# Performance work log

Measured on AMD Instinct MI355X. Metric: run time of the kernel, lower is better.

## Reference

```python
import jax, jax.numpy as jnp
import numpy as np

_CH = [(3,64),(64,64),(64,128),(128,128),(128,256),(256,256),(256,256),(256,512),(512,512),(512,512),(512,512),(512,512),(512,512)]
_RES = [32,32,16,16,8,8,8,4,4,4,2,2,2]
# (conv index, pool index applied after, or None)
_PLAN = [(0,None),(1,0),(2,None),(3,1),(4,None),(5,None),(6,2),(7,None),(8,None),(9,3),(10,None),(11,None),(12,4)]


def _bilinear(x, py, px):
    # x: [B,C,H,W]; py/px: [B,K2,H,W] float sampling coords (zero-padded outside)
    B, C, H, W = x.shape
    y0 = jnp.floor(py); x0 = jnp.floor(px)
    wy1 = (py - y0)[:, None]  # [B,1,K2,H,W]
    wx1 = (px - x0)[:, None]
    xf = x.reshape(B, C, H * W)

    def gather(yi, xi):
        valid = ((yi >= 0) & (yi < H) & (xi >= 0) & (xi < W)).astype(x.dtype)
        idx = (jnp.clip(yi, 0, H - 1) * W + jnp.clip(xi, 0, W - 1)).astype(jnp.int32)
        def gb(xb, ib, vb):
            return xb[:, ib.reshape(-1)].reshape((xb.shape[0],) + ib.shape) * vb[None]
        return jax.vmap(gb)(xf, idx, valid)  # [B,C,K2,H,W]

    g00 = gather(y0, x0); g01 = gather(y0, x0 + 1)
    g10 = gather(y0 + 1, x0); g11 = gather(y0 + 1, x0 + 1)
    return (g00 * (1 - wy1) * (1 - wx1) + g01 * (1 - wy1) * wx1
            + g10 * wy1 * (1 - wx1) + g11 * wy1 * wx1)


def _deform_conv(x, offset, w, b):
    # torchvision-style DeformConv2d, stride 1, padding 1, 3x3 kernel
    B, C, H, W = x.shape
    K = w.shape[-1]
    off = offset.reshape(B, K * K, 2, H, W)  # per kernel tap: (dy, dx)
    kk = jnp.arange(K, dtype=x.dtype) - (K // 2)
    ky = jnp.repeat(kk, K); kx = jnp.tile(kk, K)  # [K2]
    py = jnp.arange(H, dtype=x.dtype)[None, None, :, None] + ky[None, :, None, None] + off[:, :, 0]
    px = jnp.arange(W, dtype=x.dtype)[None, None, None, :] + kx[None, :, None, None] + off[:, :, 1]
    s = _bilinear(x, py, px)  # [B,C,K2,H,W]
    out = jnp.einsum('bckhw,ock->bohw', s, w.reshape(w.shape[0], C, K * K))
    return out + b[None, :, None, None]


def _bn_relu(x, g, beta):
    # training-mode BatchNorm2d (batch statistics, eps=1e-5) + ReLU
    m = jnp.mean(x, axis=(0, 2, 3), keepdims=True)
    v = jnp.mean((x - m) ** 2, axis=(0, 2, 3), keepdims=True)
    xn = (x - m) * jax.lax.rsqrt(v + 1e-5)
    return jax.nn.relu(xn * g[None, :, None, None] + beta[None, :, None, None])


def _deform_pool(x, perm, new_perm):
    # permutation-indexed 2x2 max pool: gather by perm, pool, re-permute output
    B, C, H, W = x.shape
    xp = x.reshape(B, C, H * W)[:, :, perm].reshape(B, C, H, W)
    p = xp.reshape(B, C, H // 2, 2, W // 2, 2).max(axis=(3, 5))
    return p.reshape(B, C, (H // 2) * (W // 2))[:, :, new_perm].reshape(B, C, H // 2, W // 2)


def _forward(x, offs, ws, bs, gs, betas, perms, nperms, fws, fbs):
    for ci, pi in _PLAN:
        x = _deform_conv(x, offs[ci], ws[ci], bs[ci])
        x = _bn_relu(x, gs[ci], betas[ci])
        if pi is not None:
            x = _deform_pool(x, perms[pi], nperms[pi])
    h = x.reshape(x.shape[0], -1)  # [B,512]
    h = jax.nn.relu(h @ fws[0].T + fbs[0])
    h = jax.nn.relu(h @ fws[1].T + fbs[1])
    return h @ fws[2].T + fbs[2]


def setup_inputs() -> dict:
    key = jax.random.key(0)
    ks = iter(jax.random.split(key, 128))
    B = 32
    d = {"x": jax.random.normal(next(ks), (B, 3, 32, 32), jnp.float32)}
    for i, ((ci, co), r) in enumerate(zip(_CH, _RES), 1):
        d[f"off{i}"] = jax.random.normal(next(ks), (B, 18, r, r), jnp.float32) * 0.5
        d[f"w{i}"] = jax.random.normal(next(ks), (co, ci, 3, 3), jnp.float32) * (1.0 / np.sqrt(ci * 9))
        d[f"b{i}"] = jnp.zeros((co,), jnp.float32)
        d[f"g{i}"] = jnp.ones((co,), jnp.float32)
        d[f"bb{i}"] = jnp.zeros((co,), jnp.float32)
    for i, r in enumerate([32, 16, 8, 4, 2], 1):
        d[f"perm{i}"] = jax.random.permutation(next(ks), r * r)
        d[f"nperm{i}"] = jax.random.permutation(next(ks), (r // 2) * (r // 2))
    for i, (di, do) in enumerate([(512, 4096), (4096, 4096), (4096, 100)], 1):
        d[f"fw{i}"] = jax.random.normal(next(ks), (do, di), jnp.float32) * (1.0 / np.sqrt(di))
        d[f"fb{i}"] = jnp.zeros((do,), jnp.float32)
    return d


def reference(x,
              off1, off2, off3, off4, off5, off6, off7, off8, off9, off10, off11, off12, off13,
              w1, w2, w3, w4, w5, w6, w7, w8, w9, w10, w11, w12, w13,
              b1, b2, b3, b4, b5, b6, b7, b8, b9, b10, b11, b12, b13,
              g1, g2, g3, g4, g5, g6, g7, g8, g9, g10, g11, g12, g13,
              bb1, bb2, bb3, bb4, bb5, bb6, bb7, bb8, bb9, bb10, bb11, bb12, bb13,
              perm1, perm2, perm3, perm4, perm5,
              nperm1, nperm2, nperm3, nperm4, nperm5,
              fw1, fb1, fw2, fb2, fw3, fb3):
    offs = [off1, off2, off3, off4, off5, off6, off7, off8, off9, off10, off11, off12, off13]
    ws = [w1, w2, w3, w4, w5, w6, w7, w8, w9, w10, w11, w12, w13]
    bs = [b1, b2, b3, b4, b5, b6, b7, b8, b9, b10, b11, b12, b13]
    gs = [g1, g2, g3, g4, g5, g6, g7, g8, g9, g10, g11, g12, g13]
    betas = [bb1, bb2, bb3, bb4, bb5, bb6, bb7, bb8, bb9, bb10, bb11, bb12, bb13]
    perms = [perm1, perm2, perm3, perm4, perm5]
    nperms = [nperm1, nperm2, nperm3, nperm4, nperm5]
    return _forward(x, offs, ws, bs, gs, betas, perms, nperms, [fw1, fw2, fw3], [fb1, fb2, fb3])
```

## Files before the change

### kernel.cpp

```cpp
#include <hip/hip_runtime.h>
#include <hip/hip_bf16.h>

typedef __hip_bfloat16 bf16;
typedef __attribute__((ext_vector_type(8))) short short8;
typedef __attribute__((ext_vector_type(4))) float f32x4;
typedef unsigned short u16;
#define BF2F(x) __bfloat162float(x)

__device__ __forceinline__ u16 f2bfbits(float v) {
  bf16 h = __float2bfloat16(v);
  return *(u16*)&h;
}
__device__ __forceinline__ float bfbits2f(u16 u) {
  bf16 h; *(u16*)&h = u;
  return BF2F(h);
}
__device__ __forceinline__ void splitbf(float v, u16& hi, u16& lo) {
  hi = f2bfbits(v);
  lo = f2bfbits(v - bfbits2f(hi));
}

union VecU {
  u16 u[8];
  short8 s;
};

__global__ void nchw2nhwc_kernel(const float* __restrict__ in, float* __restrict__ out,
                                 int B, int C, int HW) {
  int i = blockIdx.x * blockDim.x + threadIdx.x;
  int total = B * C * HW;
  if (i >= total) return;
  int c = i % C; int p = (i / C) % HW; int b = i / (C * HW);
  out[i] = in[((size_t)b * C + c) * HW + p];
}

template<int C, int Kp>
__device__ __forceinline__ void wtc_pair(const float* __restrict__ w, u16* __restrict__ Wh,
                                         u16* __restrict__ Wl, int rel) {
  int co = rel / C, ci = rel % C;
  const float* src = w + ((size_t)co * C + ci) * 9;
  float v[9];
#pragma unroll
  for (int k2 = 0; k2 < 9; ++k2) v[k2] = src[k2];
  size_t ob = (size_t)co * Kp + ci;
#pragma unroll
  for (int k2 = 0; k2 < 9; ++k2) {
    u16 hh, ll; splitbf(v[k2], hh, ll);
    Wh[ob + (size_t)k2 * C] = hh;
    Wl[ob + (size_t)k2 * C] = ll;
  }
}

#define PAIR_TOTAL 1634496
#define PAD_TOTAL 320

__global__ void wtc_all_v2(
    const float* w0, const float* w1, const float* w2, const float* w3,
    const float* w4, const float* w5, const float* w6, const float* w7,
    const float* w8, const float* w9, const float* w10, const float* w11,
    const float* w12, u16* __restrict__ Wh, u16* __restrict__ Wl) {
  int i = blockIdx.x * blockDim.x + threadIdx.x;
  if (i >= PAIR_TOTAL + PAD_TOTAL) return;
  if (i >= PAIR_TOTAL) {
    int t = i - PAIR_TOTAL;
    int co = t / 5, k = 27 + t % 5;
    int o = co * 32 + k;
    Wh[o] = 0; Wl[o] = 0;
    return;
  }
  if      (i < 192)     wtc_pair<3, 32>(w0, Wh + 0, Wl + 0, i);
  else if (i < 4288)    wtc_pair<64, 576>(w1, Wh + 2048, Wl + 2048, i - 192);
  else if (i < 12480)   wtc_pair<64, 576>(w2, Wh + 38912, Wl + 38912, i - 4288);
  else if (i < 28864)   wtc_pair<128, 1152>(w3, Wh + 112640, Wl + 112640, i - 12480);
  else if (i < 61632)   wtc_pair<128, 1152>(w4, Wh + 260096, Wl + 260096, i - 28864);
  else if (i < 127168)  wtc_pair<256, 2304>(w5, Wh + 555008, Wl + 555008, i - 61632);
  else if (i < 192704)  wtc_pair<256, 2304>(w6, Wh + 1144832, Wl + 1144832, i - 127168);
  else if (i < 323776)  wtc_pair<256, 2304>(w7, Wh + 1734656, Wl + 1734656, i - 192704);
  else if (i < 585920)  wtc_pair<512, 4608>(w8, Wh + 2914304, Wl + 2914304, i - 323776);
  else if (i < 848064)  wtc_pair<512, 4608>(w9, Wh + 5273600, Wl + 5273600, i - 585920);
  else if (i < 1110208) wtc_pair<512, 4608>(w10, Wh + 7632896, Wl + 7632896, i - 848064);
  else if (i < 1372352) wtc_pair<512, 4608>(w11, Wh + 9992192, Wl + 9992192, i - 1110208);
  else                  wtc_pair<512, 4608>(w12, Wh + 12351488, Wl + 12351488, i - 1372352);
}

__global__ void act_convert(const float* __restrict__ x,
                            u16* __restrict__ Ah, u16* __restrict__ Al, int total) {
  int i = blockIdx.x * blockDim.x + threadIdx.x;
  if (i >= total) return;
  u16 hh, ll; splitbf(x[i], hh, ll);
  Ah[i] = hh; Al[i] = ll;
}

__global__ __launch_bounds__(256) void deform_sample_scalar(
    const float* __restrict__ act, const float* __restrict__ off,
    u16* __restrict__ Sh, u16* __restrict__ Sl,
    int m0, int Mc, int B, int H, int W, int C, int Kp) {
  int i = blockIdx.x * blockDim.x + threadIdx.x;
  int total = Mc * Kp;
  if (i >= total) return;
  int kp = i % Kp;
  int ml = i / Kp;
  float val = 0.f;
  int K = 9 * C;
  if (kp < K) {
    int c = kp % C; int k2 = kp / C;
    int m = m0 + ml;
    int HW = H * W;
    int b = m / HW; int p = m - b * HW; int y = p / W; int x = p - y * W;
    size_t ob = (size_t)b * 18 * HW + p;
    float dy = off[ob + (size_t)(2 * k2) * HW];
    float dx = off[ob + (size_t)(2 * k2 + 1) * HW];
    float py = (float)(y + k2 / 3 - 1) + dy;
    float px = (float)(x + k2 % 3 - 1) + dx;
    float y0f = floorf(py), x0f = floorf(px);
    float wy = py - y0f, wx = px - x0f;
    int iy0 = (int)y0f, ix0 = (int)x0f;
    int iy1 = iy0 + 1, ix1 = ix0 + 1;
    float w00 = (1.f - wy) * (1.f - wx), w01 = (1.f - wy) * wx;
    float w10 = wy * (1.f - wx), w11 = wy * wx;
    if (iy0 < 0 || iy0 >= H) { w00 = 0.f; w01 = 0.f; }
    if (iy1 < 0 || iy1 >= H) { w10 = 0.f; w11 = 0.f; }
    if (ix0 < 0 || ix0 >= W) { w00 = 0.f; w10 = 0.f; }
    if (ix1 < 0 || ix1 >= W) { w01 = 0.f; w11 = 0.f; }
    int cy0 = min(max(iy0, 0), H - 1), cy1 = min(max(iy1, 0), H - 1);
    int cx0 = min(max(ix0, 0), W - 1), cx1 = min(max(ix1, 0), W - 1);
    size_t rowb = (size_t)b * HW;
    float v00 = act[(rowb + cy0 * W + cx0) * C + c];
    float v01 = act[(rowb + cy0 * W + cx1) * C + c];
    float v10 = act[(rowb + cy1 * W + cx0) * C + c];
    float v11 = act[(rowb + cy1 * W + cx1) * C + c];
    val = w00 * v00 + w01 * v01 + w10 * v10 + w11 * v11;
  }
  u16 hh, ll; splitbf(val, hh, ll);
  size_t base = (size_t)ml * Kp + kp;
  Sh[base] = hh; Sl[base] = ll;
}

#define LDA 40

__global__ __launch_bounds__(256) void mfma_gemm_tiled(
    const u16* __restrict__ Ah, const u16* __restrict__ Al,
    const u16* __restrict__ Bh, const u16* __restrict__ Bl,
    float* __restrict__ Cf, int M, int N, int Kp, int kPerZ, int splitMode) {
  __shared__ __align__(16) u16 lds[2 * 4 * 64 * LDA];
  const int TS = 64 * LDA;
  const int BS = 4 * TS;
  int tid = threadIdx.x;
  int lane = tid & 63, wave = tid >> 6;
  int l15 = lane & 15, quad = lane >> 4;
  int wr = wave >> 1, wc = wave & 1;
  int m0 = blockIdx.x * 64, n0 = blockIdx.y * 64;
  int kStart = blockIdx.z * kPerZ;
  int kEnd = min(Kp, kStart + kPerZ);
  int nSteps = (kEnd - kStart) >> 5;

  int sr = tid >> 2, sc = (tid & 3) << 3;
  const u16* gAh = Ah + (size_t)(m0 + sr) * Kp + kStart + sc;
  const u16* gAl = Al + (size_t)(m0 + sr) * Kp + kStart + sc;
  const u16* gBh = Bh + (size_t)(n0 + sr) * Kp + kStart + sc;
  const u16* gBl = Bl + (size_t)(n0 + sr) * Kp + kStart + sc;
  int soff = sr * LDA + sc;

  f32x4 z4 = {0.f, 0.f, 0.f, 0.f};
  f32x4 acc00 = z4, acc01 = z4, acc10 = z4, acc11 = z4;

  {
    short8 a = *(const short8*)gAh;
    short8 b = *(const short8*)gAl;
    short8 c = *(const short8*)gBh;
    short8 d = *(const short8*)gBl;
    *(short8*)&lds[0 * TS + soff] = a;
    *(short8*)&lds[1 * TS + soff] = b;
    *(short8*)&lds[2 * TS + soff] = c;
    *(short8*)&lds[3 * TS + soff] = d;
  }
  __syncthreads();

  int raoff = (wr * 32 + l15) * LDA + quad * 8;
  int rboff = (wc * 32 + l15) * LDA + quad * 8;

  for (int i = 0; i < nSteps; ++i) {
    int cb = (i & 1) * BS;
    bool hasNext = (i + 1 < nSteps);
    short8 nA, nB, nC, nD;
    if (hasNext) {
      int kn = (i + 1) << 5;
      nA = *(const short8*)(gAh + kn);
      nB = *(const short8*)(gAl + kn);
      nC = *(const short8*)(gBh + kn);
      nD = *(const short8*)(gBl + kn);
    }
    short8 ah0 = *(const short8*)&lds[cb + 0 * TS + raoff];
    short8 ah1 = *(const short8*)&lds[cb + 0 * TS + raoff + 16 * LDA];
    short8 al0 = *(const short8*)&lds[cb + 1 * TS + raoff];
    short8 al1 = *(const short8*)&lds[cb + 1 * TS + raoff + 16 * LDA];
    short8 bh0 = *(const short8*)&lds[cb + 2 * TS + rboff];
    short8 bh1 = *(const short8*)&lds[cb + 2 * TS + rboff + 16 * LDA];
    short8 bl0 = *(const short8*)&lds[cb + 3 * TS + rboff];
    short8 bl1 = *(const short8*)&lds[cb + 3 * TS + rboff + 16 * LDA];
    acc00 = __builtin_amdgcn_mfma_f32_16x16x32_bf16(ah0, bh0, acc00, 0, 0, 0);
    acc01 = __builtin_amdgcn_mfma_f32_16x16x32_bf16(ah0, bh1, acc01, 0, 0, 0);
    acc10 = __builtin_amdgcn_mfma_f32_16x16x32_bf16(ah1, bh0, acc10, 0, 0, 0);
    acc11 = __builtin_amdgcn_mfma_f32_16x16x32_bf16(ah1, bh1, acc11, 0, 0, 0);
    acc00 = __builtin_amdgcn_mfma_f32_16x16x32_bf16(ah0, bl0, acc00, 0, 0, 0);
    acc01 = __builtin_amdgcn_mfma_f32_16x16x32_bf16(ah0, bl1, acc01, 0, 0, 0);
    acc10 = __builtin_amdgcn_mfma_f32_16x16x32_bf16(ah1, bl0, acc10, 0, 0, 0);
    acc11 = __builtin_amdgcn_mfma_f32_16x16x32_bf16(ah1, bl1, acc11, 0, 0, 0);
    acc00 = __builtin_amdgcn_mfma_f32_16x16x32_bf16(al0, bh0, acc00, 0, 0, 0);
    acc01 = __builtin_amdgcn_mfma_f32_16x16x32_bf16(al0, bh1, acc01, 0, 0, 0);
    acc10 = __builtin_amdgcn_mfma_f32_16x16x32_bf16(al1, bh0, acc10, 0, 0, 0);
    acc11 = __builtin_amdgcn_mfma_f32_16x16x32_bf16(al1, bh1, acc11, 0, 0, 0);
    if (hasNext) {
      int ob = cb ^ BS;
      *(short8*)&lds[ob + 0 * TS + soff] = nA;
      *(short8*)&lds[ob + 1 * TS + soff] = nB;
      *(short8*)&lds[ob + 2 * TS + soff] = nC;
      *(short8*)&lds[ob + 3 * TS + soff] = nD;
      __syncthreads();
    }
  }

  float* out = Cf + (splitMode ? (size_t)blockIdx.z * M * N : (size_t)0);
  f32x4 av[2][2] = {{acc00, acc01}, {acc10, acc11}};
#pragma unroll
  for (int t = 0; t < 2; ++t) {
    int mB = m0 + wr * 32 + t * 16 + (quad << 2);
#pragma unroll
    for (int u = 0; u < 2; ++u) {
      int n = n0 + wc * 32 + u * 16 + l15;
      f32x4 a = av[t][u];
#pragma unroll
      for (int reg = 0; reg < 4; ++reg) {
        int m = mB + reg;
        out[(size_t)m * N + n] = a[reg];
      }
    }
  }
}

__global__ __launch_bounds__(256) void mfma_gemm_fused(
    const float* __restrict__ act, const float* __restrict__ stp, int bnmode,
    const float* __restrict__ off,
    const u16* __restrict__ Bh, const u16* __restrict__ Bl,
    float* __restrict__ Cf, int M, int N, int Kp, int kPerZ, int splitMode,
    int H, int W, int C, int lc, int lhw, int lw) {
  __shared__ __align__(16) u16 lds[2 * 4 * 64 * LDA];
  const int TS = 64 * LDA;
  const int BS = 4 * TS;
  int tid = threadIdx.x;
  int lane = tid & 63, wave = tid >> 6;
  int l15 = lane & 15, quad = lane >> 4;
  int wr = wave >> 1, wc = wave & 1;
  int m0 = blockIdx.x * 64, n0 = blockIdx.y * 64;
  int kStart = blockIdx.z * kPerZ;
  int kEnd = min(Kp, kStart + kPerZ);
  int nSteps = (kEnd - kStart) >> 5;

  int sr = tid >> 2, sc = (tid & 3) << 3;
  int HWv = H * W;
  int m = m0 + sr;
  int b = m >> lhw; int p = m & (HWv - 1); int y = p >> lw; int x = p & (W - 1);
  size_t obase = (size_t)b * 18 * HWv + p;
  size_t rowb = (size_t)b * HWv;
  const u16* gBh = Bh + (size_t)(n0 + sr) * Kp + kStart + sc;
  const u16* gBl = Bl + (size_t)(n0 + sr) * Kp + kStart + sc;
  int soff = sr * LDA + sc;

  f32x4 z4 = {0.f, 0.f, 0.f, 0.f};
  f32x4 acc00 = z4, acc01 = z4, acc10 = z4, acc11 = z4;

  auto SAMPLE = [&](int kk, short8& uh8, short8& ul8) {
    int k2 = kk >> lc;
    int ci = kk & (C - 1);
    float dy = off[obase + (size_t)(2 * k2) * HWv];
    float dx = off[obase + (size_t)(2 * k2 + 1) * HWv];
    float py = (float)(y + k2 / 3 - 1) + dy;
    float px = (float)(x + k2 % 3 - 1) + dx;
    float y0f = floorf(py), x0f = floorf(px);
    float wy = py - y0f, wx = px - x0f;
    int iy0 = (int)y0f, ix0 = (int)x0f;
    int iy1 = iy0 + 1, ix1 = ix0 + 1;
    float w00 = (1.f - wy) * (1.f - wx), w01 = (1.f - wy) * wx;
    float w10 = wy * (1.f - wx), w11 = wy * wx;
    if (iy0 < 0 || iy0 >= H) { w00 = 0.f; w01 = 0.f; }
    if (iy1 < 0 || iy1 >= H) { w10 = 0.f; w11 = 0.f; }
    if (ix0 < 0 || ix0 >= W) { w00 = 0.f; w10 = 0.f; }
    if (ix1 < 0 || ix1 >= W) { w01 = 0.f; w11 = 0.f; }
    int cy0 = min(max(iy0, 0), H - 1), cy1 = min(max(iy1, 0), H - 1);
    int cx0 = min(max(ix0, 0), W - 1), cx1 = min(max(ix1, 0), W - 1);
    const float* p00 = act + (rowb + cy0 * W + cx0) * C + ci;
    const float* p01 = act + (rowb + cy0 * W + cx1) * C + ci;
    const float* p10 = act + (rowb + cy1 * W + cx0) * C + ci;
    const float* p11 = act + (rowb + cy1 * W + cx1) * C + ci;
    float4 a00 = *(const float4*)p00, b00 = *(const float4*)(p00 + 4);
    float4 a01 = *(const float4*)p01, b01 = *(const float4*)(p01 + 4);
    float4 a10 = *(const float4*)p10, b10 = *(const float4*)(p10 + 4);
    float4 a11 = *(const float4*)p11, b11 = *(const float4*)(p11 + 4);
    float v00[8] = {a00.x, a00.y, a00.z, a00.w, b00.x, b00.y, b00.z, b00.w};
    float v01[8] = {a01.x, a01.y, a01.z, a01.w, b01.x, b01.y, b01.z, b01.w};
    float v10[8] = {a10.x, a10.y, a10.z, a10.w, b10.x, b10.y, b10.z, b10.w};
    float v11[8] = {a11.x, a11.y, a11.z, a11.w, b11.x, b11.y, b11.z, b11.w};
    if (bnmode) {
      float4 s0 = *(const float4*)(stp + ci), s1 = *(const float4*)(stp + ci + 4);
      float4 h0 = *(const float4*)(stp + 512 + ci), h1 = *(const float4*)(stp + 512 + ci + 4);
      float scv[8] = {s0.x, s0.y, s0.z, s0.w, s1.x, s1.y, s1.z, s1.w};
      float shv[8] = {h0.x, h0.y, h0.z, h0.w, h1.x, h1.y, h1.z, h1.w};
#pragma unroll
      for (int j = 0; j < 8; ++j) {
        v00[j] = fmaxf(v00[j] * scv[j] + shv[j], 0.f);
        v01[j] = fmaxf(v01[j] * scv[j] + shv[j], 0.f);
        v10[j] = fmaxf(v10[j] * scv[j] + shv[j], 0.f);
        v11[j] = fmaxf(v11[j] * scv[j] + shv[j], 0.f);
      }
    }
    VecU uh, ul;
#pragma unroll
    for (int j = 0; j < 8; ++j) {
      float r = w00 * v00[j] + w01 * v01[j] + w10 * v10[j] + w11 * v11[j];
      splitbf(r, uh.u[j], ul.u[j]);
    }
    uh8 = uh.s; ul8 = ul.s;
  };

  {
    short8 sa, sb;
    SAMPLE(kStart + sc, sa, sb);
    short8 c = *(const short8*)gBh;
    short8 d = *(const short8*)gBl;
    *(short8*)&lds[0 * TS + soff] = sa;
    *(short8*)&lds[1 * TS + soff] = sb;
    *(short8*)&lds[2 * TS + soff] = c;
    *(short8*)&lds[3 * TS + soff] = d;
  }
  __syncthreads();

  int raoff = (wr * 32 + l15) * LDA + quad * 8;
  int rboff = (wc * 32 + l15) * LDA + quad * 8;

  for (int i = 0; i < nSteps; ++i) {
    int cb = (i & 1) * BS;
    bool hasNext = (i + 1 < nSteps);
    short8 nA, nB, nC, nD;
    if (hasNext) {
      int kn = (i + 1) << 5;
      SAMPLE(kStart + kn + sc, nA, nB);
      nC = *(const short8*)(gBh + kn);
      nD = *(const short8*)(gBl + kn);
    }
    short8 ah0 = *(const short8*)&lds[cb + 0 * TS + raoff];
    short8 ah1 = *(const short8*)&lds[cb + 0 * TS + raoff + 16 * LDA];
    short8 al0 = *(const short8*)&lds[cb + 1 * TS + raoff];
    short8 al1 = *(const short8*)&lds[cb + 1 * TS + raoff + 16 * LDA];
    short8 bh0 = *(const short8*)&lds[cb + 2 * TS + rboff];
    short8 bh1 = *(const short8*)&lds[cb + 2 * TS + rboff + 16 * LDA];
    short8 bl0 = *(const short8*)&lds[cb + 3 * TS + rboff];
    short8 bl1 = *(const short8*)&lds[cb + 3 * TS + rboff + 16 * LDA];
    acc00 = __builtin_amdgcn_mfma_f32_16x16x32_bf16(ah0, bh0, acc00, 0, 0, 0);
    acc01 = __builtin_amdgcn_mfma_f32_16x16x32_bf16(ah0, bh1, acc01, 0, 0, 0);
    acc10 = __builtin_amdgcn_mfma_f32_16x16x32_bf16(ah1, bh0, acc10, 0, 0, 0);
    acc11 = __builtin_amdgcn_mfma_f32_16x16x32_bf16(ah1, bh1, acc11, 0, 0, 0);
    acc00 = __builtin_amdgcn_mfma_f32_16x16x32_bf16(ah0, bl0, acc00, 0, 0, 0);
    acc01 = __builtin_amdgcn_mfma_f32_16x16x32_bf16(ah0, bl1, acc01, 0, 0, 0);
    acc10 = __builtin_amdgcn_mfma_f32_16x16x32_bf16(ah1, bl0, acc10, 0, 0, 0);
    acc11 = __builtin_amdgcn_mfma_f32_16x16x32_bf16(ah1, bl1, acc11, 0, 0, 0);
    acc00 = __builtin_amdgcn_mfma_f32_16x16x32_bf16(al0, bh0, acc00, 0, 0, 0);
    acc01 = __builtin_amdgcn_mfma_f32_16x16x32_bf16(al0, bh1, acc01, 0, 0, 0);
    acc10 = __builtin_amdgcn_mfma_f32_16x16x32_bf16(al1, bh0, acc10, 0, 0, 0);
    acc11 = __builtin_amdgcn_mfma_f32_16x16x32_bf16(al1, bh1, acc11, 0, 0, 0);
    if (hasNext) {
      int ob = cb ^ BS;
      *(short8*)&lds[ob + 0 * TS + soff] = nA;
      *(short8*)&lds[ob + 1 * TS + soff] = nB;
      *(short8*)&lds[ob + 2 * TS + soff] = nC;
      *(short8*)&lds[ob + 3 * TS + soff] = nD;
      __syncthreads();
    }
  }

  float* out = Cf + (splitMode ? (size_t)blockIdx.z * M * N : (size_t)0);
  f32x4 av[2][2] = {{acc00, acc01}, {acc10, acc11}};
#pragma unroll
  for (int t = 0; t < 2; ++t) {
    int mB = m0 + wr * 32 + t * 16 + (quad << 2);
#pragma unroll
    for (int u = 0; u < 2; ++u) {
      int n = n0 + wc * 32 + u * 16 + l15;
      f32x4 a = av[t][u];
#pragma unroll
      for (int reg = 0; reg < 4; ++reg) {
        int mm = mB + reg;
        out[(size_t)mm * N + n] = a[reg];
      }
    }
  }
}

#define LDAF 40

__global__ __launch_bounds__(256) void mfma_gemm_fc4(
    const u16* __restrict__ Ah, const u16* __restrict__ Al,
    const float* __restrict__ Bw, float* __restrict__ Cf,
    int N, int K, int kPerZ) {
  __shared__ __align__(16) u16 sB[2][2][64 * LDAF];
  int tid = threadIdx.x;
  int lane = tid & 63, wave = tid >> 6;
  int l15 = lane & 15, quad = lane >> 4;
  int wm = wave >> 1, wn = wave & 1;
  int n0 = blockIdx.y * 64;
  int kStart = blockIdx.z * kPerZ;
  int kEnd = min(K, kStart + kPerZ);
  int nSteps = (kEnd - kStart) >> 5;

  int sr = tid >> 2, sc = (tid & 3) << 3;
  int gn = n0 + sr; if (gn >= N) gn = 0;
  const float* gB = Bw + (size_t)gn * K + kStart + sc;
  int soff = sr * LDAF + sc;

  const u16* pa = Ah + (size_t)(wm * 16 + l15) * K + kStart + (quad << 3);
  const u16* qa = Al + (size_t)(wm * 16 + l15) * K + kStart + (quad << 3);

  f32x4 z4 = {0.f, 0.f, 0.f, 0.f};
  f32x4 acc0 = z4, acc1 = z4;

  {
    float4 x0 = *(const float4*)gB;
    float4 x1 = *(const float4*)(gB + 4);
    float f[8] = {x0.x, x0.y, x0.z, x0.w, x1.x, x1.y, x1.z, x1.w};
    VecU uh, ul;
#pragma unroll
    for (int j = 0; j < 8; ++j) splitbf(f[j], uh.u[j], ul.u[j]);
    *(short8*)&sB[0][0][soff] = uh.s;
    *(short8*)&sB[0][1][soff] = ul.s;
  }
  __syncthreads();

  int rb0 = (wn * 32 + l15) * LDAF + (quad << 3);
  int rb1 = (wn * 32 + 16 + l15) * LDAF + (quad << 3);

  for (int i = 0; i < nSteps; ++i) {
    int cb = i & 1;
    bool hasNext = (i + 1 < nSteps);
    float4 x0, x1;
    if (hasNext) {
      int kn = (i + 1) << 5;
      x0 = *(const float4*)(gB + kn);
      x1 = *(const float4*)(gB + kn + 4);
    }
    int k0 = i << 5;
    short8 ah = *(const short8*)(pa + k0);
    short8 al = *(const short8*)(qa + k0);
    short8 bh0 = *(const short8*)&sB[cb][0][rb0];
    short8 bh1 = *(const short8*)&sB[cb][0][rb1];
    short8 bl0 = *(const short8*)&sB[cb][1][rb0];
    short8 bl1 = *(const short8*)&sB[cb][1][rb1];
    acc0 = __builtin_amdgcn_mfma_f32_16x16x32_bf16(ah, bh0, acc0, 0, 0, 0);
    acc1 = __builtin_amdgcn_mfma_f32_16x16x32_bf16(ah, bh1, acc1, 0, 0, 0);
    acc0 = __builtin_amdgcn_mfma_f32_16x16x32_bf16(ah, bl0, acc0, 0, 0, 0);
    acc1 = __builtin_amdgcn_mfma_f32_16x16x32_bf16(ah, bl1, acc1, 0, 0, 0);
    acc0 = __builtin_amdgcn_mfma_f32_16x16x32_bf16(al, bh0, acc0, 0, 0, 0);
    acc1 = __builtin_amdgcn_mfma_f32_16x16x32_bf16(al, bh1, acc1, 0, 0, 0);
    if (hasNext) {
      float f[8] = {x0.x, x0.y, x0.z, x0.w, x1.x, x1.y, x1.z, x1.w};
      VecU uh, ul;
#pragma unroll
      for (int j = 0; j < 8; ++j) splitbf(f[j], uh.u[j], ul.u[j]);
      *(short8*)&sB[cb ^ 1][0][soff] = uh.s;
      *(short8*)&sB[cb ^ 1][1][soff] = ul.s;
      __syncthreads();
    }
  }

  float* out = Cf + (size_t)blockIdx.z * 32 * N;
  f32x4 av[2] = {acc0, acc1};
#pragma unroll
  for (int u = 0; u < 2; ++u) {
    int n = n0 + wn * 32 + u * 16 + l15;
    if (n >= N) continue;
    f32x4 a = av[u];
#pragma unroll
    for (int reg = 0; reg < 4; ++reg) {
      int m = wm * 16 + (quad << 2) + reg;
      out[(size_t)m * N + n] = a[reg];
    }
  }
}

__global__ void fc_reduce_convert(const float* __restrict__ P, const float* __restrict__ bias,
                                  u16* __restrict__ Ah, u16* __restrict__ Al,
                                  int MN, int N, int zs) {
  int i = blockIdx.x * blockDim.x + threadIdx.x;
  if (i >= MN) return;
  float s = 0.f;
  for (int z = 0; z < zs; ++z) s += P[(size_t)z * MN + i];
  s += bias[i % N];
  if (s < 0.f) s = 0.f;
  u16 hh, ll; splitbf(s, hh, ll);
  Ah[i] = hh; Al[i] = ll;
}

__global__ void fc_reduce_out(const float* __restrict__ P, const float* __restrict__ bias,
                              float* __restrict__ out, int MN, int N, int zs) {
  int i = blockIdx.x * blockDim.x + threadIdx.x;
  if (i >= MN) return;
  float s = 0.f;
  for (int z = 0; z < zs; ++z) s += P[(size_t)z * MN + i];
  out[i] = s + bias[i % N];
}

__global__ __launch_bounds__(256) void bn_stats_fused(
    const float* __restrict__ P, float* __restrict__ out, float* __restrict__ st,
    const float* __restrict__ g, const float* __restrict__ bb,
    int M, int C, int rowsPerBlock, int nBlocks, int zs, int writeOut) {
  __shared__ float sh[512];
  __shared__ int isLast;
  size_t MN = (size_t)M * C;
  int t = threadIdx.x;
  int r0 = blockIdx.x * rowsPerBlock;
  int r1 = min(M, r0 + rowsPerBlock);
  if (C >= 256) {
    for (int c = t; c < C; c += 256) {
      float s = 0.f, ss = 0.f;
      for (int r = r0; r < r1; ++r) {
        size_t idx = (size_t)r * C + c;
        float v = P[idx];
        for (int z = 1; z < zs; ++z) v += P[(size_t)z * MN + idx];
        if (writeOut) out[idx] = v;
        s += v; ss += v * v;
      }
      atomicAdd(&st[c], s); atomicAdd(&st[512 + c], ss);
    }
  } else {
    int rpb = 256 / C;
    int c = t % C; int ro = t / C;
    float s = 0.f, ss = 0.f;
    for (int r = r0 + ro; r < r1; r += rpb) {
      size_t idx = (size_t)r * C + c;
      float v = P[idx];
      for (int z = 1; z < zs; ++z) v += P[(size_t)z * MN + idx];
      if (writeOut) out[idx] = v;
      s += v; ss += v * v;
    }
    sh[t] = s; sh[256 + t] = ss;
    __syncthreads();
    if (ro == 0) {
      for (int k = 1; k < rpb; ++k) { s += sh[k * C + c]; ss += sh[256 + k * C + c]; }
      atomicAdd(&st[c], s); atomicAdd(&st[512 + c], ss);
    }
  }
  __syncthreads();
  if (t == 0) {
    __threadfence();
    unsigned old = atomicAdd((unsigned int*)(st + 2048), 1u);
    isLast = (old == (unsigned)(nBlocks - 1)) ? 1 : 0;
  }
  __syncthreads();
  if (isLast) {
    for (int c = t; c < C; c += 256) {
      float s = atomicAdd(&st[c], 0.f);
      float ss = atomicAdd(&st[512 + c], 0.f);
      float mean = s / (float)M;
      float var = ss / (float)M - mean * mean;
      if (var < 0.f) var = 0.f;
      float inv = 1.0f / sqrtf(var + 1e-5f);
      float scv = g[c] * inv;
      st[1024 + c] = scv;
      st[1536 + c] = bb[c] - mean * scv;
    }
  }
}

__global__ void pool_kernel(const float* __restrict__ in, const float* __restrict__ stp,
                            float* __restrict__ out,
                            const int* __restrict__ perm, const int* __restrict__ nperm,
                            int B, int H, int C, int total) {
  int i = blockIdx.x * blockDim.x + threadIdx.x;
  if (i >= total) return;
  int oH = H / 2; int oHW = oH * oH; int HW = H * H;
  int c = i % C; int j = (i / C) % oHW; int b = i / (C * oHW);
  float sc = stp[c], sh = stp[512 + c];
  int q = min(max(nperm[j], 0), oHW - 1);
  int qy = q / oH, qx = q % oH;
  float m = 0.f;
#pragma unroll
  for (int dy = 0; dy < 2; ++dy)
#pragma unroll
    for (int dx = 0; dx < 2; ++dx) {
      int p = min(max(perm[(2 * qy + dy) * H + (2 * qx + dx)], 0), HW - 1);
      float v = in[((size_t)b * HW + p) * C + c];
      v = fmaxf(v * sc + sh, 0.f);
      m = fmaxf(m, v);
    }
  out[((size_t)b * oHW + j) * C + c] = m;
}

static inline void pick_split4(int gx, int gy, int Kp, int& zs, int& kPerZ) {
  int gxy = gx * gy;
  zs = 1;
  if (gxy < 512) {
    zs = (512 + gxy - 1) / gxy;
    int maxz = Kp / 32; if (maxz < 1) maxz = 1;
    if (zs > maxz) zs = maxz;
  }
  kPerZ = (((Kp + zs - 1) / zs) + 31) & ~31;
  zs = (Kp + kPerZ - 1) / kPerZ;
}

static inline void pick_splitFC(int gy, int K, int& zs, int& kPerZ) {
  zs = (512 + gy - 1) / gy;
  int maxz = K / 32; if (maxz < 1) maxz = 1;
  if (zs > maxz) zs = maxz;
  if (zs > 32) zs = 32;
  kPerZ = (((K + zs - 1) / zs) + 31) & ~31;
  zs = (K + kPerZ - 1) / kPerZ;
}

static inline int ilog2(int v) { int l = 0; while ((1 << l) < v) ++l; return l; }

extern "C" void kernel_launch(void* const* d_in, const int* in_sizes, int n_in,
                              void* d_out, int out_size, void* d_ws, size_t ws_size,
                              hipStream_t stream) {
  const int Ci[13]  = {3, 64, 64, 128, 128, 256, 256, 256, 512, 512, 512, 512, 512};
  const int CoA[13] = {64, 64, 128, 128, 256, 256, 256, 512, 512, 512, 512, 512, 512};
  const int Rr[13]  = {32, 32, 16, 16, 8, 8, 8, 4, 4, 4, 2, 2, 2};
  const int poolAfter[13] = {-1, 0, -1, 1, -1, -1, 2, -1, -1, 3, -1, -1, 4};
  const size_t wOff[13] = {0, 2048, 38912, 112640, 260096, 555008, 1144832, 1734656,
                           2914304, 5273600, 7632896, 9992192, 12351488};
  const int WT_TOTAL = 14710784;
  const int B = 32;
  const int ST = 2304;

  size_t cursor = 0;
  auto alloc = [&](size_t bytes) {
    void* p = (char*)d_ws + cursor;
    cursor += (bytes + 255) & ~(size_t)255;
    return p;
  };
  float* stats = (float*)alloc((size_t)13 * ST * 4);
  u16*   fcPh  = (u16*)alloc((size_t)32 * 4096 * 2);
  u16*   fcPl  = (u16*)alloc((size_t)32 * 4096 * 2);
  float* A0    = (float*)alloc((size_t)2097152 * 4);
  float* A1    = (float*)alloc((size_t)2097152 * 4);
  u16*   WTh   = (u16*)alloc((size_t)WT_TOTAL * 2);
  u16*   WTl   = (u16*)alloc((size_t)WT_TOTAL * 2);
  float* Pbuf  = (float*)alloc((size_t)4194304 * 4);
  u16*   Sh    = (u16*)alloc((size_t)1048576 * 2);
  u16*   Sl    = (u16*)alloc((size_t)1048576 * 2);
  (void)in_sizes; (void)n_in; (void)out_size;

  hipMemsetAsync(stats, 0, (size_t)13 * ST * 4, stream);

  {
    int total = B * 3 * 1024;
    nchw2nhwc_kernel<<<(total + 255) / 256, 256, 0, stream>>>(
        (const float*)d_in[0], A0, B, 3, 1024);
  }
  wtc_all_v2<<<(PAIR_TOTAL + PAD_TOTAL + 255) / 256, 256, 0, stream>>>(
      (const float*)d_in[2],  (const float*)d_in[7],  (const float*)d_in[12],
      (const float*)d_in[17], (const float*)d_in[22], (const float*)d_in[27],
      (const float*)d_in[32], (const float*)d_in[37], (const float*)d_in[42],
      (const float*)d_in[47], (const float*)d_in[52], (const float*)d_in[57],
      (const float*)d_in[62], WTh, WTl);

  float* cur = A0;
  float* oth = A1;
  int needBN = 0;
  float* stp = nullptr;

  for (int l = 0; l < 13; ++l) {
    int C = Ci[l], N = CoA[l], H = Rr[l];
    int M = B * H * H, K = 9 * C, Kp = (K + 31) & ~31;
    const float* offp = (const float*)d_in[1 + l * 5 + 0];
    const float* gp   = (const float*)d_in[1 + l * 5 + 3];
    const float* bbp  = (const float*)d_in[1 + l * 5 + 4];
    float* st = stats + (size_t)l * ST;

    int gx = M / 64, gy = N / 64;
    int zs, kPerZ;
    pick_split4(gx, gy, Kp, zs, kPerZ);
    float* gemmOut = (zs > 1) ? Pbuf : oth;

    if (l == 0) {
      int work = M * Kp;
      deform_sample_scalar<<<(work + 255) / 256, 256, 0, stream>>>(
          cur, offp, Sh, Sl, 0, M, B, H, H, C, Kp);
      mfma_gemm_tiled<<<dim3(gx, gy, zs), 256, 0, stream>>>(
          Sh, Sl, WTh + wOff[l], WTl + wOff[l], gemmOut, M, N, Kp, kPerZ, zs > 1 ? 1 : 0);
    } else {
      int lw_ = ilog2(H), lhw_ = 2 * lw_, lc_ = ilog2(C);
      mfma_gemm_fused<<<dim3(gx, gy, zs), 256, 0, stream>>>(
          cur, stp, needBN, offp, WTh + wOff[l], WTl + wOff[l],
          gemmOut, M, N, Kp, kPerZ, zs > 1 ? 1 : 0, H, H, C, lc_, lhw_, lw_);
    }

    int rowsPer = M / 128;
    if (rowsPer < 1) rowsPer = 1;
    if (rowsPer > 64) rowsPer = 64;
    int nB = (M + rowsPer - 1) / rowsPer;
    if (zs > 1)
      bn_stats_fused<<<nB, 256, 0, stream>>>(Pbuf, oth, st, gp, bbp,
                                             M, N, rowsPer, nB, zs, 1);
    else
      bn_stats_fused<<<nB, 256, 0, stream>>>(oth, oth, st, gp, bbp,
                                             M, N, rowsPer, nB, 1, 0);

    if (poolAfter[l] >= 0) {
      int pi = poolAfter[l];
      const int* perm  = (const int*)d_in[66 + pi * 2];
      const int* nperm = (const int*)d_in[66 + pi * 2 + 1];
      int oH = H / 2;
      int total = B * oH * oH * N;
      pool_kernel<<<(total + 255) / 256, 256, 0, stream>>>(oth, st + 1024, cur,
                                                           perm, nperm, B, H, N, total);
      needBN = 0; stp = nullptr;
    } else {
      float* t = cur; cur = oth; oth = t;
      needBN = 1; stp = st + 1024;
    }
  }

  const float* fw1 = (const float*)d_in[76]; const float* fb1 = (const float*)d_in[77];
  const float* fw2 = (const float*)d_in[78]; const float* fb2 = (const float*)d_in[79];
  const float* fw3 = (const float*)d_in[80]; const float* fb3 = (const float*)d_in[81];
  {
    int zs, kPerZ;
    act_convert<<<(32 * 512 + 255) / 256, 256, 0, stream>>>(cur, fcPh, fcPl, 32 * 512);
    pick_splitFC(64, 512, zs, kPerZ);
    mfma_gemm_fc4<<<dim3(1, 64, zs), 256, 0, stream>>>(fcPh, fcPl, fw1, Pbuf,
                                                       4096, 512, kPerZ);
    fc_reduce_convert<<<(32 * 4096 + 255) / 256, 256, 0, stream>>>(
        Pbuf, fb1, fcPh, fcPl, 32 * 4096, 4096, zs);
    pick_splitFC(64, 4096, zs, kPerZ);
    mfma_gemm_fc4<<<dim3(1, 64, zs), 256, 0, stream>>>(fcPh, fcPl, fw2, Pbuf,
                                                       4096, 4096, kPerZ);
    fc_reduce_convert<<<(32 * 4096 + 255) / 256, 256, 0, stream>>>(
        Pbuf, fb2, fcPh, fcPl, 32 * 4096, 4096, zs);
    pick_splitFC(2, 4096, zs, kPerZ);
    mfma_gemm_fc4<<<dim3(1, 2, zs), 256, 0, stream>>>(fcPh, fcPl, fw3, Pbuf,
                                                      100, 4096, kPerZ);
    fc_reduce_out<<<(3200 + 255) / 256, 256, 0, stream>>>(
        Pbuf, fb3, (float*)d_out, 3200, 100, zs);
  }
}
```

Baseline: 958.9 us.

## Materialize deformable samples once per layer instead of recomputing in fused GEMM

Adds a vectorized deform sampling kernel that applies pending BN+ReLU, does bilinear interpolation for 8 channels per thread, and writes split bf16 hi/lo im2col buffers. When the GEMM grid has more than one N-tile or a K split, layers now materialize samples once and run the plain tiled GEMM, rather than having every N-tile/split block resample inside the fused GEMM. This removes redundant gather work but adds a large intermediate buffer write/read and an extra launch.

Result: faster. 898.4 us (-6.3%).

```diff
diff --git a/kernel.cpp b/kernel.cpp
--- a/kernel.cpp
+++ b/kernel.cpp
@@ -89,6 +89,76 @@
   if (i >= total) return;
   u16 hh, ll; splitbf(x[i], hh, ll);
   Ah[i] = hh; Al[i] = ll;
+}
+
+__global__ __launch_bounds__(256) void deform_sample_v3(
+    const float* __restrict__ act, const float* __restrict__ stp, int bnmode,
+    const float* __restrict__ off, u16* __restrict__ Sh, u16* __restrict__ Sl,
+    int m0, int Mc, int B, int H, int W, int C, int Kp) {
+  int i = blockIdx.x * blockDim.x + threadIdx.x;
+  int c8n = C >> 3;
+  int total = Mc * 9 * c8n;
+  if (i >= total) return;
+  int c8 = i % c8n;
+  int t = i / c8n;
+  int k2 = t % 9;
+  int ml = t / 9;
+  int m = m0 + ml;
+  int HW = H * W;
+  int b = m / HW; int p = m - b * HW; int y = p / W; int x = p - y * W;
+  size_t ob = (size_t)b * 18 * HW + p;
+  float dy = off[ob + (size_t)(2 * k2) * HW];
+  float dx = off[ob + (size_t)(2 * k2 + 1) * HW];
+  float py = (float)(y + k2 / 3 - 1) + dy;
+  float px = (float)(x + k2 % 3 - 1) + dx;
+  float y0f = floorf(py), x0f = floorf(px);
+  float wy = py - y0f, wx = px - x0f;
+  int iy0 = (int)y0f, ix0 = (int)x0f;
+  int iy1 = iy0 + 1, ix1 = ix0 + 1;
+  float w00 = (1.f - wy) * (1.f - wx), w01 = (1.f - wy) * wx;
+  float w10 = wy * (1.f - wx), w11 = wy * wx;
+  if (iy0 < 0 || iy0 >= H) { w00 = 0.f; w01 = 0.f; }
+  if (iy1 < 0 || iy1 >= H) { w10 = 0.f; w11 = 0.f; }
+  if (ix0 < 0 || ix0 >= W) { w00 = 0.f; w10 = 0.f; }
+  if (ix1 < 0 || ix1 >= W) { w01 = 0.f; w11 = 0.f; }
+  int cy0 = min(max(iy0, 0), H - 1), cy1 = min(max(iy1, 0), H - 1);
+  int cx0 = min(max(ix0, 0), W - 1), cx1 = min(max(ix1, 0), W - 1);
+  int c = c8 << 3;
+  size_t rowb = (size_t)b * HW;
+  const float* p00 = act + (rowb + cy0 * W + cx0) * C + c;
+  const float* p01 = act + (rowb + cy0 * W + cx1) * C + c;
+  const float* p10 = act + (rowb + cy1 * W + cx0) * C + c;
+  const float* p11 = act + (rowb + cy1 * W + cx1) * C + c;
+  float4 a00 = *(const float4*)p00, b00 = *(const float4*)(p00 + 4);
+  float4 a01 = *(const float4*)p01, b01 = *(const float4*)(p01 + 4);
+  float4 a10 = *(const float4*)p10, b10 = *(const float4*)(p10 + 4);
+  float4 a11 = *(const float4*)p11, b11 = *(const float4*)(p11 + 4);
+  float v00[8] = {a00.x, a00.y, a00.z, a00.w, b00.x, b00.y, b00.z, b00.w};
+  float v01[8] = {a01.x, a01.y, a01.z, a01.w, b01.x, b01.y, b01.z, b01.w};
+  float v10[8] = {a10.x, a10.y, a10.z, a10.w, b10.x, b10.y, b10.z, b10.w};
+  float v11[8] = {a11.x, a11.y, a11.z, a11.w, b11.x, b11.y, b11.z, b11.w};
+  if (bnmode) {
+    float4 s0 = *(const float4*)(stp + c), s1 = *(const float4*)(stp + c + 4);
+    float4 h0 = *(const float4*)(stp + 512 + c), h1 = *(const float4*)(stp + 512 + c + 4);
+    float sc[8] = {s0.x, s0.y, s0.z, s0.w, s1.x, s1.y, s1.z, s1.w};
+    float sh[8] = {h0.x, h0.y, h0.z, h0.w, h1.x, h1.y, h1.z, h1.w};
+#pragma unroll
+    for (int j = 0; j < 8; ++j) {
+      v00[j] = fmaxf(v00[j] * sc[j] + sh[j], 0.f);
+      v01[j] = fmaxf(v01[j] * sc[j] + sh[j], 0.f);
+      v10[j] = fmaxf(v10[j] * sc[j] + sh[j], 0.f);
+      v11[j] = fmaxf(v11[j] * sc[j] + sh[j], 0.f);
+    }
+  }
+  VecU uh, ul;
+#pragma unroll
+  for (int j = 0; j < 8; ++j) {
+    float r = w00 * v00[j] + w01 * v01[j] + w10 * v10[j] + w11 * v11[j];
+    splitbf(r, uh.u[j], ul.u[j]);
+  }
+  size_t base = (size_t)ml * Kp + (size_t)k2 * C + c;
+  *(short8*)(Sh + base) = uh.s;
+  *(short8*)(Sl + base) = ul.s;
 }
 
 __global__ __launch_bounds__(256) void deform_sample_scalar(
@@ -643,8 +713,8 @@
   u16*   WTh   = (u16*)alloc((size_t)WT_TOTAL * 2);
   u16*   WTl   = (u16*)alloc((size_t)WT_TOTAL * 2);
   float* Pbuf  = (float*)alloc((size_t)4194304 * 4);
-  u16*   Sh    = (u16*)alloc((size_t)1048576 * 2);
-  u16*   Sl    = (u16*)alloc((size_t)1048576 * 2);
+  u16*   Sh    = (u16*)alloc((size_t)9437184 * 2);
+  u16*   Sl    = (u16*)alloc((size_t)9437184 * 2);
   (void)in_sizes; (void)n_in; (void)out_size;
 
   hipMemsetAsync(stats, 0, (size_t)13 * ST * 4, stream);
@@ -685,11 +755,17 @@
           cur, offp, Sh, Sl, 0, M, B, H, H, C, Kp);
       mfma_gemm_tiled<<<dim3(gx, gy, zs), 256, 0, stream>>>(
           Sh, Sl, WTh + wOff[l], WTl + wOff[l], gemmOut, M, N, Kp, kPerZ, zs > 1 ? 1 : 0);
-    } else {
+    } else if (gy == 1 && zs == 1) {
       int lw_ = ilog2(H), lhw_ = 2 * lw_, lc_ = ilog2(C);
       mfma_gemm_fused<<<dim3(gx, gy, zs), 256, 0, stream>>>(
           cur, stp, needBN, offp, WTh + wOff[l], WTl + wOff[l],
-          gemmOut, M, N, Kp, kPerZ, zs > 1 ? 1 : 0, H, H, C, lc_, lhw_, lw_);
+          gemmOut, M, N, Kp, kPerZ, 0, H, H, C, lc_, lhw_, lw_);
+    } else {
+      int work = M * 9 * (C >> 3);
+      deform_sample_v3<<<(work + 255) / 256, 256, 0, stream>>>(
+          cur, stp, needBN, offp, Sh, Sl, 0, M, B, H, H, C, Kp);
+      mfma_gemm_tiled<<<dim3(gx, gy, zs), 256, 0, stream>>>(
+          Sh, Sl, WTh + wOff[l], WTl + wOff[l], gemmOut, M, N, Kp, kPerZ, zs > 1 ? 1 : 0);
     }
 
     int rowsPer = M / 128;
```
